# Performance work log

Hardware: AMD Instinct MI355X
Metric: run time of the kernel (lower is better)

## Reference

```python
import jax, jax.numpy as jnp
import numpy as np

B, QL, H, HKV, D, MAX_SEQ = 16, 32, 32, 8, 128, 8192
CACHE_LEN = 4064  # tokens already in cache before this step
SCALE = 1.0 / np.sqrt(D).astype(np.float32)


def setup_inputs() -> dict:
    key = jax.random.key(0)
    ks = jax.random.split(key, 5)
    return {
        "q": jax.random.normal(ks[0], (B, QL, H, D), jnp.float32),
        "k": jax.random.normal(ks[1], (B, QL, HKV, D), jnp.float32),
        "v": jax.random.normal(ks[2], (B, QL, HKV, D), jnp.float32),
        "k_cache": jax.random.normal(ks[3], (B, MAX_SEQ, HKV, D), jnp.float32),
        "v_cache": jax.random.normal(ks[4], (B, MAX_SEQ, HKV, D), jnp.float32),
        "cache_seq_len": CACHE_LEN,
    }


def _attention(q, k_full, v_full):
    # q: [B, QL, H, D]; k_full/v_full: [B, KV, HKV, D]. GQA via head grouping
    # (equivalent to repeat_interleave on kv heads, without materializing it).
    rep = H // HKV
    kv_len = k_full.shape[1]
    qr = q.reshape(B, QL, HKV, rep, D)
    scores = jnp.einsum('bqhrd,bkhd->bhrqk', qr, k_full) * SCALE
    # causal mask: position j masked for query i when j > kv_len - QL + i
    mask = jnp.triu(jnp.ones((QL, kv_len), bool), k=kv_len - QL + 1)
    scores = jnp.where(mask, -jnp.inf, scores)
    weights = jax.nn.softmax(scores, axis=-1)
    out = jnp.einsum('bhrqk,bkhd->bqhrd', weights, v_full)
    return out.reshape(B, QL, H, D)


def reference(q, k, v, k_cache, v_cache, cache_seq_len):
    new_len = cache_seq_len + QL  # python int -> static slice
    k_cache = jax.lax.dynamic_update_slice(k_cache, k, (0, cache_seq_len, 0, 0))
    v_cache = jax.lax.dynamic_update_slice(v_cache, v, (0, cache_seq_len, 0, 0))
    k_full = k_cache[:, :new_len]
    v_full = v_cache[:, :new_len]
    return _attention(q, k_full, v_full)
```

## Files before the change

### kernel.cpp

```cpp
#include <hip/hip_runtime.h>

typedef unsigned short ushort_t;
typedef ushort_t ushort4v __attribute__((ext_vector_type(4)));
typedef ushort_t ushort8 __attribute__((ext_vector_type(8)));
typedef __bf16 bf16x8 __attribute__((ext_vector_type(8)));
typedef float f32x4 __attribute__((ext_vector_type(4)));

#define B_      16
#define QL_     32
#define H_      32
#define HKV_    8
#define D_      128
#define MAXSEQ_ 8192
#define REP_    4
#define ROWS_   128
#define KT_     64
#define NT_     512
#define KS_LD   136
#define VT_LD   72
#define PS_LD   72
#define NROWS_TOT (B_*HKV_*ROWS_)
#define KVSTRIDE (HKV_*D_)

template<int NSPLIT, bool DIRECT>
__global__ __launch_bounds__(NT_, 4)
void fa_main(const float* __restrict__ qg, const float* __restrict__ kg,
             const float* __restrict__ vg, const float* __restrict__ kcg,
             const float* __restrict__ vcg, const int* __restrict__ cslp,
             float* __restrict__ outg, float* __restrict__ opart,
             float* __restrict__ mpart, float* __restrict__ lpart)
{
  __shared__ __align__(16) ushort_t Ks[KT_ * KS_LD];
  __shared__ __align__(16) ushort_t Vt[D_ * VT_LD];
  __shared__ __align__(16) ushort_t Ps[8 * 16 * PS_LD];

  const int t    = threadIdx.x;
  const int s    = (int)blockIdx.x % NSPLIT;
  const int bh   = (int)blockIdx.x / NSPLIT;
  const int b    = bh / HKV_;
  const int h    = bh % HKV_;
  const int cl   = cslp[0];
  const int kvlen = cl + QL_;
  const int ntiles = (kvlen + KT_ - 1) / KT_;
  const int tps  = (ntiles + NSPLIT - 1) / NSPLIT;
  const int tt0  = s * tps;
  const int tt1  = min(ntiles, tt0 + tps);

  const int lane = t & 63;
  const int w    = t >> 6;
  const int lr   = lane & 15;
  const int lg   = lane >> 4;
  const int m0   = w * 16;

  const float qscale = 0.088388347648318447f * 1.4426950408889634f;
  bf16x8 aQ[4];
  {
    const int row = m0 + lr;
    const float* src = qg + (((size_t)b*QL_ + (row & 31))*H_ + h*REP_ + (row >> 5))*D_;
    #pragma unroll
    for (int kk = 0; kk < 4; ++kk) {
      const float* p = src + kk*32 + lg*8;
      f32x4 v0 = *(const f32x4*)(p);
      f32x4 v1 = *(const f32x4*)(p + 4);
      bf16x8 u;
      u[0]=(__bf16)(v0[0]*qscale); u[1]=(__bf16)(v0[1]*qscale);
      u[2]=(__bf16)(v0[2]*qscale); u[3]=(__bf16)(v0[3]*qscale);
      u[4]=(__bf16)(v1[0]*qscale); u[5]=(__bf16)(v1[1]*qscale);
      u[6]=(__bf16)(v1[2]*qscale); u[7]=(__bf16)(v1[3]*qscale);
      aQ[kk] = u;
    }
  }

  f32x4 oacc[8];
  #pragma unroll
  for (int nd = 0; nd < 8; ++nd) oacc[nd] = (f32x4){0.f, 0.f, 0.f, 0.f};
  float m_run = -INFINITY;
  float l_run = 0.f;
  const int q_mine = (m0 + lr) & 31;

  const int k_kl = t >> 3;
  const int k_d0 = (t & 7) * 16;
  const int v_key = t & 63;
  const int v_d0  = (t >> 6) * 16;

  const float* kc_base = kcg + ((size_t)b*MAXSEQ_*HKV_ + h)*D_ + k_d0;
  const float* kn_base = kg  + ((size_t)b*QL_*HKV_ + h)*D_ + k_d0;
  const float* vc_base = vcg + ((size_t)b*MAXSEQ_*HKV_ + h)*D_ + v_d0;
  const float* vn_base = vg  + ((size_t)b*QL_*HKV_ + h)*D_ + v_d0;

  ushort_t* PsW = Ps + w * 16 * PS_LD;

  f32x4 kr[4], vr[4];

  auto issue = [&](int tt) {
    const int p0 = tt * KT_;
    {
      int p = p0 + k_kl; if (p > kvlen - 1) p = kvlen - 1;
      const float* src = (p < cl) ? kc_base + (size_t)p*KVSTRIDE
                                  : kn_base + (size_t)(p - cl)*KVSTRIDE;
      #pragma unroll
      for (int j2 = 0; j2 < 4; ++j2) kr[j2] = *(const f32x4*)(src + 4*j2);
    }
    {
      int p = p0 + v_key; if (p > kvlen - 1) p = kvlen - 1;
      const float* src = (p < cl) ? vc_base + (size_t)p*KVSTRIDE
                                  : vn_base + (size_t)(p - cl)*KVSTRIDE;
      #pragma unroll
      for (int j2 = 0; j2 < 4; ++j2) vr[j2] = *(const f32x4*)(src + 4*j2);
    }
  };

  auto commit = [&]() {
    ushort8 u0, u1;
    #pragma unroll
    for (int j2 = 0; j2 < 2; ++j2) {
      #pragma unroll
      for (int e = 0; e < 4; ++e) {
        u0[j2*4+e] = __builtin_bit_cast(ushort_t, (__bf16)kr[j2][e]);
        u1[j2*4+e] = __builtin_bit_cast(ushort_t, (__bf16)kr[2+j2][e]);
      }
    }
    *(ushort8*)&Ks[k_kl*KS_LD + k_d0]     = u0;
    *(ushort8*)&Ks[k_kl*KS_LD + k_d0 + 8] = u1;
    #pragma unroll
    for (int j2 = 0; j2 < 4; ++j2)
      #pragma unroll
      for (int e = 0; e < 4; ++e)
        Vt[(v_d0 + j2*4 + e)*VT_LD + v_key] =
            __builtin_bit_cast(ushort_t, (__bf16)vr[j2][e]);
  };

  if (tt0 < tt1) { issue(tt0); commit(); }
  __syncthreads();

  for (int tt = tt0; tt < tt1; ++tt) {
    const bool hasNext = (tt + 1 < tt1);
    if (hasNext) issue(tt + 1);

    const int p0 = tt * KT_;

    f32x4 sacc[4];
    #pragma unroll
    for (int ni = 0; ni < 4; ++ni) {
      sacc[ni] = (f32x4){0.f, 0.f, 0.f, 0.f};
      #pragma unroll
      for (int kk = 0; kk < 4; ++kk) {
        bf16x8 ak = __builtin_bit_cast(bf16x8,
            *(const ushort8*)&Ks[(ni*16 + lr)*KS_LD + kk*32 + lg*8]);
        sacc[ni] = __builtin_amdgcn_mfma_f32_16x16x32_bf16(ak, aQ[kk], sacc[ni], 0, 0, 0);
      }
    }

    if (p0 + KT_ - 1 > cl) {
      #pragma unroll
      for (int ni = 0; ni < 4; ++ni) {
        #pragma unroll
        for (int j = 0; j < 4; ++j)
          if (p0 + ni*16 + lg*4 + j > cl + q_mine) sacc[ni][j] = -INFINITY;
      }
    }

    float tm = sacc[0][0];
    #pragma unroll
    for (int ni = 0; ni < 4; ++ni)
      #pragma unroll
      for (int j = 0; j < 4; ++j) tm = fmaxf(tm, sacc[ni][j]);
    tm = fmaxf(tm, __shfl_xor(tm, 16, 64));
    tm = fmaxf(tm, __shfl_xor(tm, 32, 64));

    if (__any(tm > m_run + 11.5f)) {
      const float mn    = fmaxf(m_run, tm);
      const float alpha = exp2f(m_run - mn);
      m_run = mn;
      l_run *= alpha;
      #pragma unroll
      for (int j = 0; j < 4; ++j) {
        const float aj = __shfl(alpha, lg*4 + j, 64);
        #pragma unroll
        for (int nd = 0; nd < 8; ++nd) oacc[nd][j] *= aj;
      }
    }

    float rs = 0.f;
    #pragma unroll
    for (int ni = 0; ni < 4; ++ni)
      #pragma unroll
      for (int j = 0; j < 4; ++j) {
        const float e = exp2f(sacc[ni][j] - m_run);
        sacc[ni][j] = e;
        rs += e;
      }
    rs += __shfl_xor(rs, 16, 64);
    rs += __shfl_xor(rs, 32, 64);
    l_run += rs;

    #pragma unroll
    for (int ni = 0; ni < 4; ++ni) {
      ushort4v u;
      #pragma unroll
      for (int j = 0; j < 4; ++j)
        u[j] = __builtin_bit_cast(ushort_t, (__bf16)sacc[ni][j]);
      *(ushort4v*)&PsW[lr*PS_LD + ni*16 + lg*4] = u;
    }

    #pragma unroll
    for (int kb = 0; kb < 2; ++kb) {
      bf16x8 ap = __builtin_bit_cast(bf16x8,
          *(const ushort8*)&PsW[lr*PS_LD + kb*32 + lg*8]);
      #pragma unroll
      for (int nd = 0; nd < 8; ++nd) {
        bf16x8 bv = __builtin_bit_cast(bf16x8,
            *(const ushort8*)&Vt[(nd*16 + lr)*VT_LD + kb*32 + lg*8]);
        oacc[nd] = __builtin_amdgcn_mfma_f32_16x16x32_bf16(ap, bv, oacc[nd], 0, 0, 0);
      }
    }

    __syncthreads();
    if (hasNext) commit();
    __syncthreads();
  }

  if constexpr (DIRECT) {
    float linv[4];
    #pragma unroll
    for (int j = 0; j < 4; ++j) {
      const float lj = __shfl(l_run, lg*4 + j, 64);
      linv[j] = (lj > 0.f) ? 1.f / lj : 0.f;
    }
    #pragma unroll
    for (int j = 0; j < 4; ++j) {
      const int row = m0 + lg*4 + j;
      float* dst = outg + (((size_t)b*QL_ + (row & 31))*H_ + h*REP_ + (row >> 5))*D_;
      #pragma unroll
      for (int nd = 0; nd < 8; ++nd) dst[nd*16 + lr] = oacc[nd][j] * linv[j];
    }
  } else {
    #pragma unroll
    for (int j = 0; j < 4; ++j) {
      const int row = m0 + lg*4 + j;
      const int R = bh * ROWS_ + row;
      float* dst = opart + ((size_t)s*NROWS_TOT + R)*D_;
      #pragma unroll
      for (int nd = 0; nd < 8; ++nd) dst[nd*16 + lr] = oacc[nd][j];
    }
    if (lane < 16) {
      const int R = bh * ROWS_ + m0 + lane;
      mpart[s*NROWS_TOT + R] = m_run;
      lpart[s*NROWS_TOT + R] = l_run;
    }
  }
}

template<int NS>
__global__ void fa_combine(const float* __restrict__ opart,
                           const float* __restrict__ mpart,
                           const float* __restrict__ lpart,
                           float* __restrict__ outg)
{
  const int idx = (int)blockIdx.x * 256 + (int)threadIdx.x;
  const int R = idx >> 7;
  const int d = idx & 127;
  float mm = -INFINITY;
  #pragma unroll
  for (int si = 0; si < NS; ++si) mm = fmaxf(mm, mpart[si*NROWS_TOT + R]);
  float L = 0.f, o = 0.f;
  #pragma unroll
  for (int si = 0; si < NS; ++si) {
    const float ms = mpart[si*NROWS_TOT + R];
    const float wgt = (ms == -INFINITY) ? 0.f : exp2f(ms - mm);
    L += lpart[si*NROWS_TOT + R] * wgt;
    o += opart[((size_t)si*NROWS_TOT + R)*D_ + d] * wgt;
  }
  const float res = (L > 0.f) ? o / L : 0.f;
  const int b   = R >> 10;
  const int h   = (R >> 7) & 7;
  const int row = R & 127;
  outg[(((size_t)b*QL_ + (row & 31))*H_ + h*REP_ + (row >> 5))*D_ + d] = res;
}

extern "C" void kernel_launch(void* const* d_in, const int* in_sizes, int n_in,
                              void* d_out, int out_size, void* d_ws, size_t ws_size,
                              hipStream_t stream)
{
  const float* qg  = (const float*)d_in[0];
  const float* kg  = (const float*)d_in[1];
  const float* vg  = (const float*)d_in[2];
  const float* kcg = (const float*)d_in[3];
  const float* vcg = (const float*)d_in[4];
  const int*   csl = (const int*)d_in[5];
  float* outg = (float*)d_out;

  const size_t need4 = (size_t)4 * NROWS_TOT * (D_ + 2) * sizeof(float);
  const size_t need2 = (size_t)2 * NROWS_TOT * (D_ + 2) * sizeof(float);
  if (ws_size >= need4) {
    float* opart = (float*)d_ws;
    float* mpart = opart + (size_t)4 * NROWS_TOT * D_;
    float* lpart = mpart + 4 * NROWS_TOT;
    hipLaunchKernelGGL((fa_main<4, false>), dim3(4 * B_ * HKV_), dim3(NT_), 0, stream,
                       qg, kg, vg, kcg, vcg, csl, nullptr, opart, mpart, lpart);
    hipLaunchKernelGGL((fa_combine<4>), dim3(NROWS_TOT * D_ / 256), dim3(256), 0, stream,
                       opart, mpart, lpart, outg);
  } else if (ws_size >= need2) {
    float* opart = (float*)d_ws;
    float* mpart = opart + (size_t)2 * NROWS_TOT * D_;
    float* lpart = mpart + 2 * NROWS_TOT;
    hipLaunchKernelGGL((fa_main<2, false>), dim3(2 * B_ * HKV_), dim3(NT_), 0, stream,
                       qg, kg, vg, kcg, vcg, csl, nullptr, opart, mpart, lpart);
    hipLaunchKernelGGL((fa_combine<2>), dim3(NROWS_TOT * D_ / 256), dim3(256), 0, stream,
                       opart, mpart, lpart, outg);
  } else {
    hipLaunchKernelGGL((fa_main<1, true>), dim3(B_ * HKV_), dim3(NT_), 0, stream,
                       qg, kg, vg, kcg, vcg, csl, outg, nullptr, nullptr, nullptr);
  }
}
```

Baseline: 151.2 us.

## Switch attention to 32x32x16 MFMA with register-resident P via permlane swap

Moves both the QK^T and PV products from 16x16x32 to 32x32x16 bf16 MFMA, with each wave owning one head's 32 query rows. The softmax probabilities are repacked in registers using v_permlane32_swap instead of going through the shared-memory P buffer, which removes that LDS round trip and its buffer. Block size drops to 256 threads, launch bounds change to 2 blocks, and the K/V staging is remapped so V transposes are written as packed pairs. The aim is fewer LDS operations and shuffles per tile. The cost is higher register pressure and fewer threads per block for the global loads.

```diff
diff --git a/kernel.cpp b/kernel.cpp
--- a/kernel.cpp
+++ b/kernel.cpp
@@ -1,10 +1,11 @@
 #include <hip/hip_runtime.h>
 
 typedef unsigned short ushort_t;
-typedef ushort_t ushort4v __attribute__((ext_vector_type(4)));
 typedef ushort_t ushort8 __attribute__((ext_vector_type(8)));
 typedef __bf16 bf16x8 __attribute__((ext_vector_type(8)));
 typedef float f32x4 __attribute__((ext_vector_type(4)));
+typedef float f32x16 __attribute__((ext_vector_type(16)));
+typedef unsigned uint4v __attribute__((ext_vector_type(4)));
 
 #define B_      16
 #define QL_     32
@@ -15,15 +16,20 @@
 #define REP_    4
 #define ROWS_   128
 #define KT_     64
-#define NT_     512
+#define NT_     256
 #define KS_LD   136
 #define VT_LD   72
-#define PS_LD   72
 #define NROWS_TOT (B_*HKV_*ROWS_)
 #define KVSTRIDE (HKV_*D_)
 
+__device__ __forceinline__ unsigned pkbf(float lo, float hi2) {
+  unsigned a  = (unsigned)__builtin_bit_cast(ushort_t, (__bf16)lo);
+  unsigned b2 = (unsigned)__builtin_bit_cast(ushort_t, (__bf16)hi2);
+  return a | (b2 << 16);
+}
+
 template<int NSPLIT, bool DIRECT>
-__global__ __launch_bounds__(NT_, 4)
+__global__ __launch_bounds__(NT_, 2)
 void fa_main(const float* __restrict__ qg, const float* __restrict__ kg,
              const float* __restrict__ vg, const float* __restrict__ kcg,
              const float* __restrict__ vcg, const int* __restrict__ cslp,
@@ -32,7 +38,6 @@
 {
   __shared__ __align__(16) ushort_t Ks[KT_ * KS_LD];
   __shared__ __align__(16) ushort_t Vt[D_ * VT_LD];
-  __shared__ __align__(16) ushort_t Ps[8 * 16 * PS_LD];
 
   const int t    = threadIdx.x;
   const int s    = (int)blockIdx.x % NSPLIT;
@@ -48,49 +53,45 @@
 
   const int lane = t & 63;
   const int w    = t >> 6;
-  const int lr   = lane & 15;
-  const int lg   = lane >> 4;
-  const int m0   = w * 16;
+  const int qcol = lane & 31;
+  const int hi   = lane >> 5;
 
   const float qscale = 0.088388347648318447f * 1.4426950408889634f;
-  bf16x8 aQ[4];
+  bf16x8 aQ[8];
   {
-    const int row = m0 + lr;
-    const float* src = qg + (((size_t)b*QL_ + (row & 31))*H_ + h*REP_ + (row >> 5))*D_;
-    #pragma unroll
-    for (int kk = 0; kk < 4; ++kk) {
-      const float* p = src + kk*32 + lg*8;
-      f32x4 v0 = *(const f32x4*)(p);
-      f32x4 v1 = *(const f32x4*)(p + 4);
+    const float* src = qg + (((size_t)b*QL_ + qcol)*H_ + h*REP_ + w)*D_ + hi*8;
+    #pragma unroll
+    for (int ks = 0; ks < 8; ++ks) {
+      f32x4 v0 = *(const f32x4*)(src + ks*16);
+      f32x4 v1 = *(const f32x4*)(src + ks*16 + 4);
       bf16x8 u;
       u[0]=(__bf16)(v0[0]*qscale); u[1]=(__bf16)(v0[1]*qscale);
       u[2]=(__bf16)(v0[2]*qscale); u[3]=(__bf16)(v0[3]*qscale);
       u[4]=(__bf16)(v1[0]*qscale); u[5]=(__bf16)(v1[1]*qscale);
       u[6]=(__bf16)(v1[2]*qscale); u[7]=(__bf16)(v1[3]*qscale);
-      aQ[kk] = u;
-    }
-  }
-
-  f32x4 oacc[8];
+      aQ[ks] = u;
+    }
+  }
+
+  f32x16 oacc[4];
   #pragma unroll
-  for (int nd = 0; nd < 8; ++nd) oacc[nd] = (f32x4){0.f, 0.f, 0.f, 0.f};
+  for (int db = 0; db < 4; ++db)
+    #pragma unroll
+    for (int r = 0; r < 16; ++r) oacc[db][r] = 0.f;
   float m_run = -INFINITY;
   float l_run = 0.f;
-  const int q_mine = (m0 + lr) & 31;
-
-  const int k_kl = t >> 3;
-  const int k_d0 = (t & 7) * 16;
-  const int v_key = t & 63;
-  const int v_d0  = (t >> 6) * 16;
-
-  const float* kc_base = kcg + ((size_t)b*MAXSEQ_*HKV_ + h)*D_ + k_d0;
-  const float* kn_base = kg  + ((size_t)b*QL_*HKV_ + h)*D_ + k_d0;
-  const float* vc_base = vcg + ((size_t)b*MAXSEQ_*HKV_ + h)*D_ + v_d0;
-  const float* vn_base = vg  + ((size_t)b*QL_*HKV_ + h)*D_ + v_d0;
-
-  ushort_t* PsW = Ps + w * 16 * PS_LD;
-
-  f32x4 kr[4], vr[4];
+
+  const int k_kl = t >> 2;
+  const int k_d0 = (t & 3) * 32;
+  const int v_k2 = (t & 31) * 2;
+  const int v_d0 = (t >> 5) * 16;
+
+  const float* kc_base = kcg + (size_t)b*MAXSEQ_*KVSTRIDE + h*D_ + k_d0;
+  const float* kn_base = kg  + (size_t)b*QL_*KVSTRIDE    + h*D_ + k_d0;
+  const float* vc_base = vcg + (size_t)b*MAXSEQ_*KVSTRIDE + h*D_ + v_d0;
+  const float* vn_base = vg  + (size_t)b*QL_*KVSTRIDE    + h*D_ + v_d0;
+
+  f32x4 kr[8], vr[8];
 
   auto issue = [&](int tt) {
     const int p0 = tt * KT_;
@@ -99,35 +100,34 @@
       const float* src = (p < cl) ? kc_base + (size_t)p*KVSTRIDE
                                   : kn_base + (size_t)(p - cl)*KVSTRIDE;
       #pragma unroll
-      for (int j2 = 0; j2 < 4; ++j2) kr[j2] = *(const f32x4*)(src + 4*j2);
-    }
-    {
-      int p = p0 + v_key; if (p > kvlen - 1) p = kvlen - 1;
+      for (int j = 0; j < 8; ++j) kr[j] = *(const f32x4*)(src + 4*j);
+    }
+    #pragma unroll
+    for (int kk = 0; kk < 2; ++kk) {
+      int p = p0 + v_k2 + kk; if (p > kvlen - 1) p = kvlen - 1;
       const float* src = (p < cl) ? vc_base + (size_t)p*KVSTRIDE
                                   : vn_base + (size_t)(p - cl)*KVSTRIDE;
       #pragma unroll
-      for (int j2 = 0; j2 < 4; ++j2) vr[j2] = *(const f32x4*)(src + 4*j2);
+      for (int j = 0; j < 4; ++j) vr[kk*4 + j] = *(const f32x4*)(src + 4*j);
     }
   };
 
   auto commit = [&]() {
-    ushort8 u0, u1;
-    #pragma unroll
-    for (int j2 = 0; j2 < 2; ++j2) {
+    #pragma unroll
+    for (int c2 = 0; c2 < 4; ++c2) {
+      ushort8 u;
       #pragma unroll
       for (int e = 0; e < 4; ++e) {
-        u0[j2*4+e] = __builtin_bit_cast(ushort_t, (__bf16)kr[j2][e]);
-        u1[j2*4+e] = __builtin_bit_cast(ushort_t, (__bf16)kr[2+j2][e]);
-      }
-    }
-    *(ushort8*)&Ks[k_kl*KS_LD + k_d0]     = u0;
-    *(ushort8*)&Ks[k_kl*KS_LD + k_d0 + 8] = u1;
-    #pragma unroll
-    for (int j2 = 0; j2 < 4; ++j2)
-      #pragma unroll
-      for (int e = 0; e < 4; ++e)
-        Vt[(v_d0 + j2*4 + e)*VT_LD + v_key] =
-            __builtin_bit_cast(ushort_t, (__bf16)vr[j2][e]);
+        u[e]   = __builtin_bit_cast(ushort_t, (__bf16)kr[c2*2][e]);
+        u[4+e] = __builtin_bit_cast(ushort_t, (__bf16)kr[c2*2+1][e]);
+      }
+      *(ushort8*)&Ks[k_kl*KS_LD + k_d0 + c2*8] = u;
+    }
+    #pragma unroll
+    for (int dj = 0; dj < 16; ++dj) {
+      const unsigned pr = pkbf(vr[dj>>2][dj&3], vr[4 + (dj>>2)][dj&3]);
+      *(unsigned*)&Vt[(v_d0 + dj)*VT_LD + v_k2] = pr;
+    }
   };
 
   if (tt0 < tt1) { issue(tt0); commit(); }
@@ -139,33 +139,34 @@
 
     const int p0 = tt * KT_;
 
-    f32x4 sacc[4];
-    #pragma unroll
-    for (int ni = 0; ni < 4; ++ni) {
-      sacc[ni] = (f32x4){0.f, 0.f, 0.f, 0.f};
-      #pragma unroll
-      for (int kk = 0; kk < 4; ++kk) {
+    f32x16 sacc[2];
+    #pragma unroll
+    for (int kg = 0; kg < 2; ++kg) {
+      #pragma unroll
+      for (int r = 0; r < 16; ++r) sacc[kg][r] = 0.f;
+      #pragma unroll
+      for (int ks = 0; ks < 8; ++ks) {
         bf16x8 ak = __builtin_bit_cast(bf16x8,
-            *(const ushort8*)&Ks[(ni*16 + lr)*KS_LD + kk*32 + lg*8]);
-        sacc[ni] = __builtin_amdgcn_mfma_f32_16x16x32_bf16(ak, aQ[kk], sacc[ni], 0, 0, 0);
+            *(const ushort8*)&Ks[(kg*32 + qcol)*KS_LD + ks*16 + hi*8]);
+        sacc[kg] = __builtin_amdgcn_mfma_f32_32x32x16_bf16(ak, aQ[ks], sacc[kg], 0, 0, 0);
       }
     }
 
     if (p0 + KT_ - 1 > cl) {
       #pragma unroll
-      for (int ni = 0; ni < 4; ++ni) {
+      for (int kg = 0; kg < 2; ++kg)
         #pragma unroll
-        for (int j = 0; j < 4; ++j)
-          if (p0 + ni*16 + lg*4 + j > cl + q_mine) sacc[ni][j] = -INFINITY;
-      }
-    }
-
-    float tm = sacc[0][0];
-    #pragma unroll
-    for (int ni = 0; ni < 4; ++ni)
-      #pragma unroll
-      for (int j = 0; j < 4; ++j) tm = fmaxf(tm, sacc[ni][j]);
-    tm = fmaxf(tm, __shfl_xor(tm, 16, 64));
+        for (int r = 0; r < 16; ++r) {
+          const int key = p0 + kg*32 + (r&3) + 8*(r>>2) + 4*hi;
+          if (key > cl + qcol) sacc[kg][r] = -INFINITY;
+        }
+    }
+
+    float tm = -INFINITY;
+    #pragma unroll
+    for (int kg = 0; kg < 2; ++kg)
+      #pragma unroll
+      for (int r = 0; r < 16; ++r) tm = fmaxf(tm, sacc[kg][r]);
     tm = fmaxf(tm, __shfl_xor(tm, 32, 64));
 
     if (__any(tm > m_run + 11.5f)) {
@@ -174,44 +175,46 @@
       m_run = mn;
       l_run *= alpha;
       #pragma unroll
-      for (int j = 0; j < 4; ++j) {
-        const float aj = __shfl(alpha, lg*4 + j, 64);
+      for (int r = 0; r < 16; ++r) {
+        const int rq = (r&3) + 8*(r>>2) + 4*hi;
+        const float ar = __shfl(alpha, rq, 64);
         #pragma unroll
-        for (int nd = 0; nd < 8; ++nd) oacc[nd][j] *= aj;
+        for (int db = 0; db < 4; ++db) oacc[db][r] *= ar;
       }
     }
 
     float rs = 0.f;
     #pragma unroll
-    for (int ni = 0; ni < 4; ++ni)
-      #pragma unroll
-      for (int j = 0; j < 4; ++j) {
-        const float e = exp2f(sacc[ni][j] - m_run);
-        sacc[ni][j] = e;
+    for (int kg = 0; kg < 2; ++kg)
+      #pragma unroll
+      for (int r = 0; r < 16; ++r) {
+        const float e = exp2f(sacc[kg][r] - m_run);
+        sacc[kg][r] = e;
         rs += e;
       }
-    rs += __shfl_xor(rs, 16, 64);
     rs += __shfl_xor(rs, 32, 64);
     l_run += rs;
 
     #pragma unroll
-    for (int ni = 0; ni < 4; ++ni) {
-      ushort4v u;
-      #pragma unroll
-      for (int j = 0; j < 4; ++j)
-        u[j] = __builtin_bit_cast(ushort_t, (__bf16)sacc[ni][j]);
-      *(ushort4v*)&PsW[lr*PS_LD + ni*16 + lg*4] = u;
-    }
-
-    #pragma unroll
-    for (int kb = 0; kb < 2; ++kb) {
-      bf16x8 ap = __builtin_bit_cast(bf16x8,
-          *(const ushort8*)&PsW[lr*PS_LD + kb*32 + lg*8]);
-      #pragma unroll
-      for (int nd = 0; nd < 8; ++nd) {
-        bf16x8 bv = __builtin_bit_cast(bf16x8,
-            *(const ushort8*)&Vt[(nd*16 + lr)*VT_LD + kb*32 + lg*8]);
-        oacc[nd] = __builtin_amdgcn_mfma_f32_16x16x32_bf16(ap, bv, oacc[nd], 0, 0, 0);
+    for (int kg = 0; kg < 2; ++kg) {
+      #pragma unroll
+      for (int hl = 0; hl < 2; ++hl) {
+        const int rb = hl * 8;
+        unsigned a0 = pkbf(sacc[kg][rb+0], sacc[kg][rb+1]);
+        unsigned b0 = pkbf(sacc[kg][rb+4], sacc[kg][rb+5]);
+        unsigned a1 = pkbf(sacc[kg][rb+2], sacc[kg][rb+3]);
+        unsigned b1 = pkbf(sacc[kg][rb+6], sacc[kg][rb+7]);
+        asm volatile("v_permlane32_swap_b32 %0, %1" : "+v"(a0), "+v"(b0));
+        asm volatile("v_permlane32_swap_b32 %0, %1" : "+v"(a1), "+v"(b1));
+        uint4v wv; wv[0] = a0; wv[1] = a1; wv[2] = b0; wv[3] = b1;
+        const bf16x8 ap = __builtin_bit_cast(bf16x8, wv);
+        const int kbase = kg*32 + hl*16;
+        #pragma unroll
+        for (int db = 0; db < 4; ++db) {
+          bf16x8 bv = __builtin_bit_cast(bf16x8,
+              *(const ushort8*)&Vt[(db*32 + qcol)*VT_LD + kbase + hi*8]);
+          oacc[db] = __builtin_amdgcn_mfma_f32_32x32x16_bf16(ap, bv, oacc[db], 0, 0, 0);
+        }
       }
     }
 
@@ -220,33 +223,28 @@
     __syncthreads();
   }
 
+  const float inv_own = (l_run > 0.f) ? 1.f / l_run : 0.f;
   if constexpr (DIRECT) {
-    float linv[4];
-    #pragma unroll
-    for (int j = 0; j < 4; ++j) {
-      const float lj = __shfl(l_run, lg*4 + j, 64);
-      linv[j] = (lj > 0.f) ? 1.f / lj : 0.f;
-    }
-    #pragma unroll
-    for (int j = 0; j < 4; ++j) {
-      const int row = m0 + lg*4 + j;
-      float* dst = outg + (((size_t)b*QL_ + (row & 31))*H_ + h*REP_ + (row >> 5))*D_;
-      #pragma unroll
-      for (int nd = 0; nd < 8; ++nd) dst[nd*16 + lr] = oacc[nd][j] * linv[j];
+    #pragma unroll
+    for (int r = 0; r < 16; ++r) {
+      const int rq = (r&3) + 8*(r>>2) + 4*hi;
+      const float inv = __shfl(inv_own, rq, 64);
+      float* dst = outg + (((size_t)b*QL_ + rq)*H_ + h*REP_ + w)*D_ + qcol;
+      #pragma unroll
+      for (int db = 0; db < 4; ++db) dst[db*32] = oacc[db][r] * inv;
     }
   } else {
-    #pragma unroll
-    for (int j = 0; j < 4; ++j) {
-      const int row = m0 + lg*4 + j;
-      const int R = bh * ROWS_ + row;
-      float* dst = opart + ((size_t)s*NROWS_TOT + R)*D_;
-      #pragma unroll
-      for (int nd = 0; nd < 8; ++nd) dst[nd*16 + lr] = oacc[nd][j];
-    }
-    if (lane < 16) {
-      const int R = bh * ROWS_ + m0 + lane;
-      mpart[s*NROWS_TOT + R] = m_run;
-      lpart[s*NROWS_TOT + R] = l_run;
+    const int R0 = bh * ROWS_ + w * 32;
+    #pragma unroll
+    for (int r = 0; r < 16; ++r) {
+      const int rq = (r&3) + 8*(r>>2) + 4*hi;
+      float* dst = opart + ((size_t)s*NROWS_TOT + R0 + rq)*D_ + qcol;
+      #pragma unroll
+      for (int db = 0; db < 4; ++db) dst[db*32] = oacc[db][r];
+    }
+    if (lane < 32) {
+      mpart[s*NROWS_TOT + R0 + lane] = m_run;
+      lpart[s*NROWS_TOT + R0 + lane] = l_run;
     }
   }
 }
```

Result: faster. 129.0 us (-14.7%).
